# Optimization experiments

Measured on AMD Instinct MI355X. Metric: run time of the kernel, lower is better.

The kernel has to match this reference:

```python
import jax, jax.numpy as jnp
import numpy as np

N = 100000      # nodes
E = 3200000     # edges (avg degree 32)
D_IN, H, D_OUT = 512, 16, 64


def setup_inputs() -> dict:
    key = jax.random.key(0)
    k = jax.random.split(key, 7)
    x = jax.random.normal(k[0], (N, D_IN), dtype=jnp.float32)
    edge_index = jax.random.randint(k[1], (2, E), 0, N, dtype=jnp.int64)
    edge_weight = jax.random.uniform(k[2], (E,), dtype=jnp.float32)
    W1 = jax.random.normal(k[3], (D_IN, H), dtype=jnp.float32) * (1.0 / np.sqrt(D_IN))
    b1 = jnp.zeros((H,), dtype=jnp.float32)
    W2 = jax.random.normal(k[4], (H, D_OUT), dtype=jnp.float32) * (1.0 / np.sqrt(H))
    b2 = jnp.zeros((D_OUT,), dtype=jnp.float32)
    return {"x": x, "edge_index": edge_index, "edge_weight": edge_weight,
            "W1": W1, "b1": b1, "W2": W2, "b2": b2}


def _gcn_conv(x, edge_index, edge_weight, W, b):
    """PyG GCNConv (normalize=True, add self-loops): D^-1/2 (A+I) D^-1/2 (x W) + b."""
    n = x.shape[0]
    src, dst = edge_index[0], edge_index[1]
    loop = jnp.arange(n, dtype=src.dtype)
    row = jnp.concatenate([src, loop])            # message source
    col = jnp.concatenate([dst, loop])            # aggregation target
    w = jnp.concatenate([edge_weight, jnp.ones((n,), x.dtype)])
    deg = jax.ops.segment_sum(w, col, num_segments=n)
    dinv = jnp.where(deg > 0, jax.lax.rsqrt(deg), 0.0)
    norm = dinv[row] * w * dinv[col]              # [E+N]
    h = x @ W                                     # linear before propagate (PyG order)
    msg = h[row] * norm[:, None]                  # gather + scale, [E+N, d_out]
    out = jax.ops.segment_sum(msg, col, num_segments=n)  # scatter-add
    return out + b


def reference(x, edge_index, edge_weight, W1, b1, W2, b2):
    h = jax.nn.relu(_gcn_conv(x, edge_index, edge_weight, W1, b1))
    # F.dropout(training=self.training): identity in eval mode
    return _gcn_conv(h, edge_index, edge_weight, W2, b2)
```

## Files before the change

kernel.cpp:

```cpp
#include <hip/hip_runtime.h>


constexpr int BKT_BITS = 8;
constexpr int BKT = 1 << BKT_BITS;
constexpr int EPB = 16384;

__global__ __launch_bounds__(256) void k_pre(
    const float* __restrict__ x, const float* __restrict__ W1,
    float* __restrict__ h1pre, int n,
    const int* __restrict__ dst, int* __restrict__ hist, int ne, int nb,
    int xw1b) {
  __shared__ float W1t[16 * 512];
  if ((int)blockIdx.x >= xw1b) {
    int* sh = (int*)W1t;
    int hb = blockIdx.x - xw1b;
    for (int i = threadIdx.x; i < nb; i += 256) sh[i] = 0;
    __syncthreads();
    int base = hb * EPB;
    int end = min(base + EPB, ne);
    for (int e = base + threadIdx.x; e < end; e += 256)
      atomicAdd(&sh[dst[e] >> BKT_BITS], 1);
    __syncthreads();
    for (int i = threadIdx.x; i < nb; i += 256) hist[hb * nb + i] = sh[i];
    return;
  }
  {
#pragma unroll
    for (int i = 0; i < 32; ++i) {
      int idx = threadIdx.x + i * 256;
      int k = idx >> 4, j = idx & 15;
      W1t[j * 512 + k] = W1[idx];
    }
  }
  __syncthreads();
  int gtid = blockIdx.x * 256 + threadIdx.x;
  int rp = gtid >> 2, q = gtid & 3;
  int r0 = rp * 2;
  if (r0 >= n) return;
  int r1 = r0 + 1;
  bool has1 = (r1 < n);
  const float4* x4 = (const float4*)x;
  const float4* W1t4 = (const float4*)W1t;
  float acc0[16], acc1[16];
#pragma unroll
  for (int j = 0; j < 16; ++j) { acc0[j] = 0.f; acc1[j] = 0.f; }
  long rb0 = (long)r0 * 128 + q;
  long rb1 = (long)r1 * 128 + q;
  for (int m = 0; m < 32; ++m) {
    float4 a = x4[rb0 + m * 4];
    float4 b = has1 ? x4[rb1 + m * 4] : make_float4(0.f, 0.f, 0.f, 0.f);
    int p = q + m * 4;
#pragma unroll
    for (int j = 0; j < 16; ++j) {
      float4 w = W1t4[j * 128 + p];
      acc0[j] = fmaf(a.x, w.x, acc0[j]);
      acc0[j] = fmaf(a.y, w.y, acc0[j]);
      acc0[j] = fmaf(a.z, w.z, acc0[j]);
      acc0[j] = fmaf(a.w, w.w, acc0[j]);
      acc1[j] = fmaf(b.x, w.x, acc1[j]);
      acc1[j] = fmaf(b.y, w.y, acc1[j]);
      acc1[j] = fmaf(b.z, w.z, acc1[j]);
      acc1[j] = fmaf(b.w, w.w, acc1[j]);
    }
  }
#pragma unroll
  for (int j = 0; j < 16; ++j) {
    acc0[j] += __shfl_xor(acc0[j], 1);
    acc0[j] += __shfl_xor(acc0[j], 2);
    acc1[j] += __shfl_xor(acc1[j], 1);
    acc1[j] += __shfl_xor(acc1[j], 2);
  }
  if (q == 0) {
    float4* o4 = (float4*)h1pre;
#pragma unroll
    for (int j4 = 0; j4 < 4; ++j4) {
      o4[(long)r0 * 4 + j4] =
          make_float4(acc0[4 * j4], acc0[4 * j4 + 1], acc0[4 * j4 + 2], acc0[4 * j4 + 3]);
      if (has1)
        o4[(long)r1 * 4 + j4] =
            make_float4(acc1[4 * j4], acc1[4 * j4 + 1], acc1[4 * j4 + 2], acc1[4 * j4 + 3]);
    }
  }
}

__global__ __launch_bounds__(256) void k_colscan(
    const int* __restrict__ hist, int* __restrict__ basep,
    int* __restrict__ colsum, int nblk, int nb) {
  __shared__ int sh[256];
  __shared__ int carry_s;
  int k = blockIdx.x;
  int t = threadIdx.x;
  if (t == 0) carry_s = 0;
  __syncthreads();
  for (int c0 = 0; c0 < nblk; c0 += 256) {
    int b = c0 + t;
    int v = (b < nblk) ? hist[b * nb + k] : 0;
    sh[t] = v;
    __syncthreads();
    for (int d = 1; d < 256; d <<= 1) {
      int u = (t >= d) ? sh[t - d] : 0;
      __syncthreads();
      sh[t] += u;
      __syncthreads();
    }
    if (b < nblk) basep[b * nb + k] = carry_s + sh[t] - v;
    __syncthreads();
    if (t == 0) carry_s += sh[255];
    __syncthreads();
  }
  if (t == 0) colsum[k] = carry_s;
}

__global__ __launch_bounds__(256) void k_scanb(
    const int* __restrict__ colsum, int* __restrict__ bstart, int nb) {
  __shared__ int sh[256];
  __shared__ int carry_s;
  int t = threadIdx.x;
  if (t == 0) carry_s = 0;
  __syncthreads();
  for (int c0 = 0; c0 < nb; c0 += 256) {
    int k = c0 + t;
    int v = (k < nb) ? colsum[k] : 0;
    sh[t] = v;
    __syncthreads();
    for (int d = 1; d < 256; d <<= 1) {
      int u = (t >= d) ? sh[t - d] : 0;
      __syncthreads();
      sh[t] += u;
      __syncthreads();
    }
    if (k < nb) bstart[k] = carry_s + sh[t] - v;
    __syncthreads();
    if (t == 0) carry_s += sh[255];
    __syncthreads();
  }
  if (t == 0) bstart[nb] = carry_s;
}

__global__ __launch_bounds__(256) void k_binfill(
    const int* __restrict__ ei, const float* __restrict__ ew,
    const int* __restrict__ basep, const int* __restrict__ bstart,
    uint2* __restrict__ recs, int ne, int nb) {
  extern __shared__ int cur[];
  for (int i = threadIdx.x; i < nb; i += 256)
    cur[i] = basep[blockIdx.x * nb + i] + bstart[i];
  __syncthreads();
  int bs = blockIdx.x * EPB;
  int end = min(bs + EPB, ne);
  for (int e = bs + threadIdx.x; e < end; e += 256) {
    int s = ei[e];
    int d = ei[ne + e];
    float w = ew[e];
    int bkt = d >> BKT_BITS;
    int pos = atomicAdd(&cur[bkt], 1);
    recs[pos] = make_uint2((unsigned)s | ((unsigned)(d & (BKT - 1)) << 20),
                           __float_as_uint(w));
  }
}

__global__ __launch_bounds__(256) void k_csr(
    const uint2* __restrict__ recs, const int* __restrict__ bstart,
    uint2* __restrict__ csr, int* __restrict__ rowptr,
    float* __restrict__ dinv, int n, int ne) {
  __shared__ float sdeg[BKT];
  __shared__ int soff[BKT];
  __shared__ int scur[BKT];
  int t = threadIdx.x;
  sdeg[t] = 0.f;
  soff[t] = 0;
  __syncthreads();
  int k = blockIdx.x;
  int s0 = bstart[k], s1 = bstart[k + 1];
  for (int e = s0 + t; e < s1; e += 256) {
    uint2 r = recs[e];
    int dl = (r.x >> 20) & (BKT - 1);
    atomicAdd(&soff[dl], 1);
    atomicAdd(&sdeg[dl], __uint_as_float(r.y));
  }
  __syncthreads();
  int v = soff[t];
  for (int d = 1; d < BKT; d <<= 1) {
    int u = (t >= d) ? soff[t - d] : 0;
    __syncthreads();
    soff[t] += u;
    __syncthreads();
  }
  int excl = soff[t] - v;
  scur[t] = excl;
  int node = (k << BKT_BITS) + t;
  if (node < n) {
    rowptr[node] = s0 + excl;
    dinv[node] = 1.0f / sqrtf(sdeg[t] + 1.0f);
  }
  if (k == 0 && t == 0) rowptr[n] = ne;
  __syncthreads();
  for (int e = s0 + t; e < s1; e += 256) {
    uint2 r = recs[e];
    int dl = (r.x >> 20) & (BKT - 1);
    int pos = s0 + atomicAdd(&scur[dl], 1);
    csr[pos] = make_uint2(r.x & 0xFFFFF, r.y);
  }
}

template <int MODE>
__global__ __launch_bounds__(256) void k_agg(
    const float* __restrict__ hin, const uint2* __restrict__ csr,
    const int* __restrict__ rowptr, const float* __restrict__ dinv,
    const float* __restrict__ bias, const float* __restrict__ W2,
    float* __restrict__ out, int n) {
  __shared__ float W2s[MODE == 2 ? 16 * 64 : 1];
  __shared__ float accs[MODE == 2 ? 256 : 1];
  if (MODE == 2) {
#pragma unroll
    for (int s = 0; s < 4; ++s) W2s[threadIdx.x + s * 256] = W2[threadIdx.x + s * 256];
  }
  int gtid = blockIdx.x * 256 + threadIdx.x;
  int node = gtid >> 4, j = gtid & 15;
  bool valid = node < n;
  float acc = 0.f;
  if (valid) {
    float dv = dinv[node];
    acc = dv * hin[(long)node * 16 + j];
    int e = rowptr[node], e1 = rowptr[node + 1];
    for (; e + 3 < e1; e += 4) {
      uint2 r0 = csr[e], r1 = csr[e + 1], r2 = csr[e + 2], r3 = csr[e + 3];
      float f0 = __uint_as_float(r0.y) * dinv[r0.x];
      float f1 = __uint_as_float(r1.y) * dinv[r1.x];
      float f2 = __uint_as_float(r2.y) * dinv[r2.x];
      float f3 = __uint_as_float(r3.y) * dinv[r3.x];
      float h0 = hin[(long)r0.x * 16 + j];
      float h1 = hin[(long)r1.x * 16 + j];
      float h2 = hin[(long)r2.x * 16 + j];
      float h3 = hin[(long)r3.x * 16 + j];
      acc = fmaf(f0, h0, acc);
      acc = fmaf(f1, h1, acc);
      acc = fmaf(f2, h2, acc);
      acc = fmaf(f3, h3, acc);
    }
    for (; e < e1; ++e) {
      uint2 r = csr[e];
      acc = fmaf(__uint_as_float(r.y) * dinv[r.x], hin[(long)r.x * 16 + j], acc);
    }
    acc *= dv;
  }
  if (MODE == 1) {
    if (valid) out[(long)node * 16 + j] = fmaxf(acc + bias[j], 0.f);
    return;
  }
  accs[threadIdx.x] = acc;
  __syncthreads();
  int nl = threadIdx.x >> 4;
  int o4 = threadIdx.x & 15;
  int node2 = blockIdx.x * 16 + nl;
  if (node2 < n) {
    const float4* W2s4 = (const float4*)W2s;
    float4 v = ((const float4*)bias)[o4];
#pragma unroll
    for (int jj = 0; jj < 16; ++jj) {
      float a = accs[nl * 16 + jj];
      float4 w = W2s4[jj * 16 + o4];
      v.x = fmaf(a, w.x, v.x);
      v.y = fmaf(a, w.y, v.y);
      v.z = fmaf(a, w.z, v.z);
      v.w = fmaf(a, w.w, v.w);
    }
    ((float4*)out)[(long)node2 * 16 + o4] = v;
  }
}

extern "C" void kernel_launch(void* const* d_in, const int* in_sizes, int n_in,
                              void* d_out, int out_size, void* d_ws, size_t ws_size,
                              hipStream_t stream) {
  const float* x  = (const float*)d_in[0];
  const int*   ei = (const int*)d_in[1];
  const float* ew = (const float*)d_in[2];
  const float* W1 = (const float*)d_in[3];
  const float* b1 = (const float*)d_in[4];
  const float* W2 = (const float*)d_in[5];
  const float* b2 = (const float*)d_in[6];
  float* out = (float*)d_out;
  int n  = in_sizes[0] / 512;
  int ne = in_sizes[1] / 2;

  int nb   = (n + BKT - 1) >> BKT_BITS;
  int nblk = (ne + EPB - 1) / EPB;

  char* ws = (char*)d_ws;
  size_t off = 0;
  auto alloc = [&](size_t bytes) {
    size_t r = off;
    off += (bytes + 255) & ~(size_t)255;
    return r;
  };
  float* dinv   = (float*)(ws + alloc((size_t)n * 4));
  float* h1pre  = (float*)(ws + alloc((size_t)n * 16 * 4));
  float* h1     = (float*)(ws + alloc((size_t)n * 16 * 4));
  uint2* recs   = (uint2*)(ws + alloc((size_t)ne * 8));
  uint2* csr    = (uint2*)(ws + alloc((size_t)ne * 8));
  int*   rowptr = (int*)  (ws + alloc((size_t)(n + 1) * 4));
  int*   hist   = (int*)  (ws + alloc((size_t)nblk * nb * 4));
  int*   basep  = (int*)  (ws + alloc((size_t)nblk * nb * 4));
  int*   colsum = (int*)  (ws + alloc((size_t)nb * 4));
  int*   bstart = (int*)  (ws + alloc((size_t)(nb + 1) * 4));
  (void)ws_size; (void)n_in; (void)out_size;

  int nrp = (n + 1) / 2;
  int xw1b = (nrp * 4 + 255) / 256;
  k_pre<<<xw1b + nblk, 256, 0, stream>>>(x, W1, h1pre, n, ei + ne, hist, ne, nb, xw1b);

  k_colscan<<<nb, 256, 0, stream>>>(hist, basep, colsum, nblk, nb);
  k_scanb<<<1, 256, 0, stream>>>(colsum, bstart, nb);
  size_t shb = (size_t)nb * 4;
  k_binfill<<<nblk, 256, shb, stream>>>(ei, ew, basep, bstart, recs, ne, nb);
  k_csr<<<nb, 256, 0, stream>>>(recs, bstart, csr, rowptr, dinv, n, ne);

  int gN16 = (n * 16 + 255) / 256;
  k_agg<1><<<gN16, 256, 0, stream>>>(h1pre, csr, rowptr, dinv, b1, nullptr, h1, n);
  k_agg<2><<<gN16, 256, 0, stream>>>(h1, csr, rowptr, dinv, b2, W2, out, n);
}
```

Measured before the change: 265.7 us.

## Prescale features by dinv and gather float4 per thread in aggregation

Features are prescaled by the source node's inverse sqrt degree: layer-1 inputs inside the CSR-build kernel, and layer-2 inputs in the layer-1 epilogue. This removes the per-edge dinv[src] random gather from both aggregation passes. The aggregation kernels also switch from 16 threads per node with scalar loads to 4 threads per node with float4 loads, cutting the repeated per-thread CSR reads. The cost is an extra read-modify-write pass over h1pre and fewer threads per node, which can expose latency on high-degree rows.

```diff
diff --git a/kernel.cpp b/kernel.cpp
--- a/kernel.cpp
+++ b/kernel.cpp
@@ -161,7 +161,7 @@
 __global__ __launch_bounds__(256) void k_csr(
     const uint2* __restrict__ recs, const int* __restrict__ bstart,
     uint2* __restrict__ csr, int* __restrict__ rowptr,
-    float* __restrict__ dinv, int n, int ne) {
+    float* __restrict__ dinv, float* __restrict__ h1pre, int n, int ne) {
   __shared__ float sdeg[BKT];
   __shared__ int soff[BKT];
   __shared__ int scur[BKT];
@@ -188,10 +188,13 @@
   int excl = soff[t] - v;
   scur[t] = excl;
   int node = (k << BKT_BITS) + t;
+  float dvv = 0.f;
   if (node < n) {
+    dvv = 1.0f / sqrtf(sdeg[t] + 1.0f);
     rowptr[node] = s0 + excl;
-    dinv[node] = 1.0f / sqrtf(sdeg[t] + 1.0f);
-  }
+    dinv[node] = dvv;
+  }
+  sdeg[t] = dvv;
   if (k == 0 && t == 0) rowptr[n] = ne;
   __syncthreads();
   for (int e = s0 + t; e < s1; e += 256) {
@@ -199,6 +202,15 @@
     int dl = (r.x >> 20) & (BKT - 1);
     int pos = s0 + atomicAdd(&scur[dl], 1);
     csr[pos] = make_uint2(r.x & 0xFFFFF, r.y);
+  }
+  int nbase = k << BKT_BITS;
+  int lim4 = (min(n - nbase, BKT)) * 4;
+  float4* h4 = (float4*)h1pre + (long)nbase * 4;
+  for (int i = t; i < lim4; i += 256) {
+    float dv2 = sdeg[i >> 2];
+    float4 hv = h4[i];
+    hv.x *= dv2; hv.y *= dv2; hv.z *= dv2; hv.w *= dv2;
+    h4[i] = hv;
   }
 }
 
@@ -209,62 +221,80 @@
     const float* __restrict__ bias, const float* __restrict__ W2,
     float* __restrict__ out, int n) {
   __shared__ float W2s[MODE == 2 ? 16 * 64 : 1];
-  __shared__ float accs[MODE == 2 ? 256 : 1];
+  __shared__ float accs[MODE == 2 ? 64 * 16 : 1];
   if (MODE == 2) {
 #pragma unroll
     for (int s = 0; s < 4; ++s) W2s[threadIdx.x + s * 256] = W2[threadIdx.x + s * 256];
   }
+  const float4* hin4 = (const float4*)hin;
   int gtid = blockIdx.x * 256 + threadIdx.x;
-  int node = gtid >> 4, j = gtid & 15;
+  int node = gtid >> 2, q = gtid & 3;
   bool valid = node < n;
-  float acc = 0.f;
+  float4 acc = make_float4(0.f, 0.f, 0.f, 0.f);
+  float dv = 0.f;
   if (valid) {
-    float dv = dinv[node];
-    acc = dv * hin[(long)node * 16 + j];
+    dv = dinv[node];
+    acc = hin4[(long)node * 4 + q];
     int e = rowptr[node], e1 = rowptr[node + 1];
     for (; e + 3 < e1; e += 4) {
       uint2 r0 = csr[e], r1 = csr[e + 1], r2 = csr[e + 2], r3 = csr[e + 3];
-      float f0 = __uint_as_float(r0.y) * dinv[r0.x];
-      float f1 = __uint_as_float(r1.y) * dinv[r1.x];
-      float f2 = __uint_as_float(r2.y) * dinv[r2.x];
-      float f3 = __uint_as_float(r3.y) * dinv[r3.x];
-      float h0 = hin[(long)r0.x * 16 + j];
-      float h1 = hin[(long)r1.x * 16 + j];
-      float h2 = hin[(long)r2.x * 16 + j];
-      float h3 = hin[(long)r3.x * 16 + j];
-      acc = fmaf(f0, h0, acc);
-      acc = fmaf(f1, h1, acc);
-      acc = fmaf(f2, h2, acc);
-      acc = fmaf(f3, h3, acc);
+      float4 h0 = hin4[(long)r0.x * 4 + q];
+      float4 h1 = hin4[(long)r1.x * 4 + q];
+      float4 h2 = hin4[(long)r2.x * 4 + q];
+      float4 h3 = hin4[(long)r3.x * 4 + q];
+      float f0 = __uint_as_float(r0.y), f1 = __uint_as_float(r1.y);
+      float f2 = __uint_as_float(r2.y), f3 = __uint_as_float(r3.y);
+      acc.x = fmaf(f0, h0.x, acc.x); acc.y = fmaf(f0, h0.y, acc.y);
+      acc.z = fmaf(f0, h0.z, acc.z); acc.w = fmaf(f0, h0.w, acc.w);
+      acc.x = fmaf(f1, h1.x, acc.x); acc.y = fmaf(f1, h1.y, acc.y);
+      acc.z = fmaf(f1, h1.z, acc.z); acc.w = fmaf(f1, h1.w, acc.w);
+      acc.x = fmaf(f2, h2.x, acc.x); acc.y = fmaf(f2, h2.y, acc.y);
+      acc.z = fmaf(f2, h2.z, acc.z); acc.w = fmaf(f2, h2.w, acc.w);
+      acc.x = fmaf(f3, h3.x, acc.x); acc.y = fmaf(f3, h3.y, acc.y);
+      acc.z = fmaf(f3, h3.z, acc.z); acc.w = fmaf(f3, h3.w, acc.w);
     }
     for (; e < e1; ++e) {
       uint2 r = csr[e];
-      acc = fmaf(__uint_as_float(r.y) * dinv[r.x], hin[(long)r.x * 16 + j], acc);
-    }
-    acc *= dv;
+      float4 h = hin4[(long)r.x * 4 + q];
+      float f = __uint_as_float(r.y);
+      acc.x = fmaf(f, h.x, acc.x); acc.y = fmaf(f, h.y, acc.y);
+      acc.z = fmaf(f, h.z, acc.z); acc.w = fmaf(f, h.w, acc.w);
+    }
+    acc.x *= dv; acc.y *= dv; acc.z *= dv; acc.w *= dv;
   }
   if (MODE == 1) {
-    if (valid) out[(long)node * 16 + j] = fmaxf(acc + bias[j], 0.f);
+    if (valid) {
+      float4 b = ((const float4*)bias)[q];
+      float4 o;
+      o.x = dv * fmaxf(acc.x + b.x, 0.f);
+      o.y = dv * fmaxf(acc.y + b.y, 0.f);
+      o.z = dv * fmaxf(acc.z + b.z, 0.f);
+      o.w = dv * fmaxf(acc.w + b.w, 0.f);
+      ((float4*)out)[(long)node * 4 + q] = o;
+    }
     return;
   }
-  accs[threadIdx.x] = acc;
-  __syncthreads();
-  int nl = threadIdx.x >> 4;
-  int o4 = threadIdx.x & 15;
-  int node2 = blockIdx.x * 16 + nl;
-  if (node2 < n) {
-    const float4* W2s4 = (const float4*)W2s;
-    float4 v = ((const float4*)bias)[o4];
-#pragma unroll
-    for (int jj = 0; jj < 16; ++jj) {
-      float a = accs[nl * 16 + jj];
-      float4 w = W2s4[jj * 16 + o4];
-      v.x = fmaf(a, w.x, v.x);
-      v.y = fmaf(a, w.y, v.y);
-      v.z = fmaf(a, w.z, v.z);
-      v.w = fmaf(a, w.w, v.w);
-    }
-    ((float4*)out)[(long)node2 * 16 + o4] = v;
+  ((float4*)accs)[threadIdx.x] = acc;
+  __syncthreads();
+  const float4* W2s4 = (const float4*)W2s;
+#pragma unroll
+  for (int it = 0; it < 4; ++it) {
+    int nl = it * 16 + (threadIdx.x >> 4);
+    int o4 = threadIdx.x & 15;
+    int node2 = blockIdx.x * 64 + nl;
+    if (node2 < n) {
+      float4 v = ((const float4*)bias)[o4];
+#pragma unroll
+      for (int jj = 0; jj < 16; ++jj) {
+        float a = accs[nl * 16 + jj];
+        float4 w = W2s4[jj * 16 + o4];
+        v.x = fmaf(a, w.x, v.x);
+        v.y = fmaf(a, w.y, v.y);
+        v.z = fmaf(a, w.z, v.z);
+        v.w = fmaf(a, w.w, v.w);
+      }
+      ((float4*)out)[(long)node2 * 16 + o4] = v;
+    }
   }
 }
 
@@ -312,9 +342,9 @@
   k_scanb<<<1, 256, 0, stream>>>(colsum, bstart, nb);
   size_t shb = (size_t)nb * 4;
   k_binfill<<<nblk, 256, shb, stream>>>(ei, ew, basep, bstart, recs, ne, nb);
-  k_csr<<<nb, 256, 0, stream>>>(recs, bstart, csr, rowptr, dinv, n, ne);
-
-  int gN16 = (n * 16 + 255) / 256;
-  k_agg<1><<<gN16, 256, 0, stream>>>(h1pre, csr, rowptr, dinv, b1, nullptr, h1, n);
-  k_agg<2><<<gN16, 256, 0, stream>>>(h1, csr, rowptr, dinv, b2, W2, out, n);
-}
+  k_csr<<<nb, 256, 0, stream>>>(recs, bstart, csr, rowptr, dinv, h1pre, n, ne);
+
+  int gN4 = (n * 4 + 255) / 256;
+  k_agg<1><<<gN4, 256, 0, stream>>>(h1pre, csr, rowptr, dinv, b1, nullptr, h1, n);
+  k_agg<2><<<gN4, 256, 0, stream>>>(h1, csr, rowptr, dinv, b2, W2, out, n);
+}
```

Result: no change. 260.7 us (-1.9%).
